# Kernel optimization log

Hardware: AMD Instinct MI355X
Metric: run time of the kernel (lower is better)

Reference implementation:

```python
import jax, jax.numpy as jnp
import numpy as np

B, T, C = 4, 2048, 1024
N_HEADS = 16
HEAD_DIM = C // N_HEADS


def setup_inputs() -> dict:
    key = jax.random.key(0)
    k1, k2, k3 = jax.random.split(key, 3)
    x = jax.random.normal(k1, (B, T, C), dtype=jnp.float32)
    w_qkv = jax.random.normal(k2, (C, 3 * C), dtype=jnp.float32) * (1.0 / np.sqrt(C))
    w_proj = jax.random.normal(k3, (C, C), dtype=jnp.float32) * (1.0 / np.sqrt(C))
    return {"x": x, "w_qkv": w_qkv, "w_proj": w_proj}


def reference(x, w_qkv, w_proj):
    b, t, c = x.shape
    qkv = x @ w_qkv                                  # [B,T,3C]
    q, k, v = jnp.split(qkv, 3, axis=-1)
    def split_heads(u):
        return u.reshape(b, t, N_HEADS, HEAD_DIM).transpose(0, 2, 1, 3)  # [B,H,T,D]
    q, k, v = split_heads(q), split_heads(k), split_heads(v)
    scale = 1.0 / np.sqrt(HEAD_DIM)
    att = jnp.einsum('bhqd,bhkd->bhqk', q, k) * scale   # [B,H,T,T]
    causal = jnp.tril(jnp.ones((t, t), dtype=bool))
    att = jnp.where(causal[None, None], att, -jnp.inf)
    att = jax.nn.softmax(att, axis=-1)
    out = jnp.einsum('bhqk,bhkd->bhqd', att, v)         # [B,H,T,D]
    out = out.transpose(0, 2, 1, 3).reshape(b, t, c)
    return out @ w_proj
```

## Files before the change

### kernel.cpp

```cpp
#include <hip/hip_runtime.h>
#include <hip/hip_bf16.h>
#include <stdint.h>

typedef __bf16 bf16_t;
typedef __bf16 bf16x4 __attribute__((ext_vector_type(4)));
typedef __bf16 bf16x8 __attribute__((ext_vector_type(8)));
typedef float  f32x4  __attribute__((ext_vector_type(4)));

#define B_    4
#define T_    2048
#define C_    1024
#define NH    16
#define HD    64
#define M_TOT (B_ * T_)

__device__ __forceinline__ void gload16(const void* g, void* l) {
    __builtin_amdgcn_global_load_lds(
        (const __attribute__((address_space(1))) uint32_t*)g,
        (__attribute__((address_space(3))) uint32_t*)l, 16, 0, 0);
}

__global__ void conv_x_kernel(const float* __restrict__ x, bf16_t* __restrict__ xb, int n4) {
    int i = blockIdx.x * blockDim.x + threadIdx.x;
    int stride = gridDim.x * blockDim.x;
    for (; i < n4; i += stride) {
        float4 v = reinterpret_cast<const float4*>(x)[i];
        union { bf16_t h[4]; uint2 u; } p;
        p.h[0] = (bf16_t)v.x; p.h[1] = (bf16_t)v.y;
        p.h[2] = (bf16_t)v.z; p.h[3] = (bf16_t)v.w;
        reinterpret_cast<uint2*>(xb)[i] = p.u;
    }
}

__global__ void transpose_w_kernel(const float* __restrict__ w, bf16_t* __restrict__ wt,
                                   int K, int N) {
    __shared__ float tile[32][33];
    int n0 = blockIdx.x * 32, k0 = blockIdx.y * 32;
    int tx = threadIdx.x, ty = threadIdx.y;
    #pragma unroll
    for (int i = 0; i < 32; i += 8)
        tile[ty + i][tx] = w[(size_t)(k0 + ty + i) * N + n0 + tx];
    __syncthreads();
    #pragma unroll
    for (int i = 0; i < 32; i += 8)
        wt[(size_t)(n0 + ty + i) * K + k0 + tx] = (bf16_t)tile[tx][ty + i];
}

#define QSCALE 0.18033688011112042f

#define LA0 0
#define LA1 16384
#define LB0 32768
#define LB1 49152

#define GST(ptr, rbase, base, kt) do { int k0_ = ((kt) << 6) & (K - 1);           \
    _Pragma("unroll") for (int c_ = 0; c_ < 4; ++c_) {                            \
        int li_ = tid + c_ * 256; int row_ = li_ >> 3;                            \
        int sw_ = (li_ & 7) ^ (row_ & 7);                                         \
        gload16(ptr + (size_t)((rbase) + row_) * K + k0_ + sw_ * 8,               \
                lds + (base) + li_ * 16); } } while (0)

#define GREAD(abase, bbase) do {                                                  \
    _Pragma("unroll") for (int mi_ = 0; mi_ < 4; ++mi_)                           \
        _Pragma("unroll") for (int kk_ = 0; kk_ < 2; ++kk_) {                     \
            int row_  = wm * 64 + mi_ * 16 + q16;                                 \
            int byte_ = (row_ * 128 + kk_ * 64 + g * 16) ^ ((row_ & 7) << 4);     \
            af[mi_ * 2 + kk_] = *reinterpret_cast<const bf16x8*>(lds + (abase) + byte_); } \
    _Pragma("unroll") for (int n_ = 0; n_ < 4; ++n_)                              \
        _Pragma("unroll") for (int kk_ = 0; kk_ < 2; ++kk_) {                     \
            int row_  = wn * 64 + n_ * 16 + q16;                                  \
            int byte_ = (row_ * 128 + kk_ * 64 + g * 16) ^ ((row_ & 7) << 4);     \
            bfr[n_ * 2 + kk_] = *reinterpret_cast<const bf16x8*>(lds + (bbase) + byte_); } } while (0)

#define GMFMA(milo) do { __builtin_amdgcn_s_setprio(1);                           \
    _Pragma("unroll") for (int mi_ = 0; mi_ < 2; ++mi_)                           \
        _Pragma("unroll") for (int kk_ = 0; kk_ < 2; ++kk_)                       \
            _Pragma("unroll") for (int n_ = 0; n_ < 4; ++n_)                      \
                acc[(milo) + mi_][n_] = __builtin_amdgcn_mfma_f32_16x16x32_bf16(  \
                    af[((milo) + mi_) * 2 + kk_], bfr[n_ * 2 + kk_],              \
                    acc[(milo) + mi_][n_], 0, 0, 0);                              \
    __builtin_amdgcn_s_setprio(0); } while (0)

template<int MODE>
__global__ __launch_bounds__(256, 2) void gemm_kernel(
    const bf16_t* __restrict__ A, const bf16_t* __restrict__ Bt,
    float* __restrict__ Cout,
    bf16_t* __restrict__ Qo, bf16_t* __restrict__ Ko, bf16_t* __restrict__ Vt,
    int M, int N, int K)
{
    __shared__ __align__(16) char lds[65536];
    const int tid  = threadIdx.x;
    const int lane = tid & 63;
    const int wid  = tid >> 6;
    const int wm   = wid >> 1, wn = wid & 1;
    const int q16  = lane & 15, g = lane >> 4;
    const int xcd = blockIdx.x & 7;
    const int i0  = blockIdx.x >> 3;
    const int mbase = (xcd * 8 + (i0 & 7)) * 128;
    const int nbase = (i0 >> 3) * 128;
    const int NITER = K >> 7;

    f32x4  acc[4][4] = {};
    bf16x8 af[8], bfr[8];

    GST(A, mbase, LA0, 0); GST(Bt, nbase, LB0, 0);
    GST(A, mbase, LA1, 1); GST(Bt, nbase, LB1, 1);
    asm volatile("s_waitcnt vmcnt(8)" ::: "memory");
    __builtin_amdgcn_s_barrier();
    __builtin_amdgcn_sched_barrier(0);

    #pragma unroll 1
    for (int i = 0; i < NITER; ++i) {
        GREAD(LA0, LB0);
        __builtin_amdgcn_s_barrier();
        asm volatile("s_waitcnt lgkmcnt(0)" ::: "memory");
        __builtin_amdgcn_sched_barrier(0);
        GMFMA(0);
        __builtin_amdgcn_s_barrier();
        GST(A, mbase, LA0, 2 * i + 2); GST(Bt, nbase, LB0, 2 * i + 2);
        __builtin_amdgcn_sched_barrier(0);
        GMFMA(2);
        asm volatile("s_waitcnt vmcnt(8)" ::: "memory");
        __builtin_amdgcn_s_barrier();
        GREAD(LA1, LB1);
        __builtin_amdgcn_s_barrier();
        asm volatile("s_waitcnt lgkmcnt(0)" ::: "memory");
        __builtin_amdgcn_sched_barrier(0);
        GMFMA(0);
        __builtin_amdgcn_s_barrier();
        GST(A, mbase, LA1, 2 * i + 3); GST(Bt, nbase, LB1, 2 * i + 3);
        __builtin_amdgcn_sched_barrier(0);
        GMFMA(2);
        asm volatile("s_waitcnt vmcnt(8)" ::: "memory");
        __builtin_amdgcn_s_barrier();
    }
    asm volatile("s_waitcnt vmcnt(0)" ::: "memory");

    #pragma unroll
    for (int mi = 0; mi < 4; ++mi) {
        #pragma unroll
        for (int n = 0; n < 4; ++n) {
            const int row0 = mbase + wm * 64 + mi * 16 + g * 4;
            const int col0 = nbase + wn * 64 + n * 16;
            if (MODE == 0) {
                #pragma unroll
                for (int r = 0; r < 4; ++r)
                    Cout[(size_t)(row0 + r) * N + col0 + q16] = acc[mi][n][r];
            } else {
                const int b = row0 >> 11, t0 = row0 & 2047;
                if (col0 < 1024) {
                    int h = col0 >> 6, d = (col0 & 63) + q16;
                    #pragma unroll
                    for (int r = 0; r < 4; ++r)
                        Qo[((size_t)(b * NH + h) * T_ + t0 + r) * HD + d] =
                            (bf16_t)(acc[mi][n][r] * QSCALE);
                } else if (col0 < 2048) {
                    int h = (col0 - 1024) >> 6, d = (col0 & 63) + q16;
                    #pragma unroll
                    for (int r = 0; r < 4; ++r)
                        Ko[((size_t)(b * NH + h) * T_ + t0 + r) * HD + d] =
                            (bf16_t)acc[mi][n][r];
                } else {
                    int h = (col0 - 2048) >> 6, d = (col0 & 63) + q16;
                    bf16x4 vv = { (bf16_t)acc[mi][n][0], (bf16_t)acc[mi][n][1],
                                  (bf16_t)acc[mi][n][2], (bf16_t)acc[mi][n][3] };
                    *reinterpret_cast<bf16x4*>(
                        Vt + ((size_t)(b * NH + h) * HD + d) * T_ + t0) = vv;
                }
            }
        }
    }
}

__global__ __launch_bounds__(256, 3) void attn_kernel(
    const bf16_t* __restrict__ Q, const bf16_t* __restrict__ K,
    const bf16_t* __restrict__ Vt, bf16_t* __restrict__ out)
{
    __shared__ __align__(16) char kvbuf[2][16384];
    __shared__ __align__(16) char plds[4][2048];
    const int tid  = threadIdx.x;
    const int lane = tid & 63;
    const int wid  = tid >> 6;
    const int g    = lane >> 4;
    const int q16  = lane & 15;

    const int bid = blockIdx.x;
    const int k   = bid >> 6;
    const int bh  = bid & 63;
    const int b   = bh >> 4, h = bh & 15;
    const int qt  = (k < 4) ? (15 - k) : (k < 8) ? (k + 4) : (k < 12) ? (k - 4) : (15 - k);

    const bf16_t* Qh = Q  + (size_t)bh * T_ * HD;
    const bf16_t* Kh = K  + (size_t)bh * T_ * HD;
    const bf16_t* Vh = Vt + (size_t)bh * HD * T_;
    char* myp = plds[wid];
    const int pswz = (q16 & 7) << 4;

    const int nt    = 2 * qt + 2;
    const int qbase = qt * 128 + wid * 32;
    const int qg0   = qbase + q16;
    const int qg1   = qbase + 16 + q16;

    int koff[4][2], pwoff[4], proff[2];
    #pragma unroll
    for (int t = 0; t < 4; ++t) {
        #pragma unroll
        for (int kk = 0; kk < 2; ++kk)
            koff[t][kk] = ((t * 16 + q16) * 128 + kk * 64 + g * 16) ^ pswz;
        pwoff[t] = (q16 * 128 + t * 32 + g * 8) ^ pswz;
    }
    proff[0] = (q16 * 128 + g * 16) ^ pswz;
    proff[1] = (q16 * 128 + 64 + g * 16) ^ pswz;

    const int li0 = tid,        row0 = li0 >> 3, sw0 = (li0 & 7) ^ (row0 & 7);
    const int li1 = tid + 256,  row1 = li1 >> 3, sw1 = (li1 & 7) ^ (row1 & 7);
    const bf16_t* kS0 = Kh + (size_t)row0 * HD + sw0 * 8;
    const bf16_t* kS1 = Kh + (size_t)row1 * HD + sw1 * 8;
    const bf16_t* vS0 = Vh + (size_t)row0 * T_ + sw0 * 8;
    const bf16_t* vS1 = Vh + (size_t)row1 * T_ + sw1 * 8;

#define STAGE2(buf) do {                                                          \
        gload16(kS0, (char*)(buf) + tid * 16);                                    \
        gload16(kS1, (char*)(buf) + 4096 + tid * 16);                             \
        gload16(vS0, (char*)(buf) + 8192 + tid * 16);                             \
        gload16(vS1, (char*)(buf) + 12288 + tid * 16);                            \
        kS0 += 4096; kS1 += 4096; vS0 += 64; vS1 += 64; } while (0)

    bf16x8 qf0[2], qf1[2];
    #pragma unroll
    for (int kk = 0; kk < 2; ++kk) {
        qf0[kk] = *reinterpret_cast<const bf16x8*>(Qh + (size_t)qg0 * HD + kk * 32 + g * 8);
        qf1[kk] = *reinterpret_cast<const bf16x8*>(Qh + (size_t)qg1 * HD + kk * 32 + g * 8);
    }

    f32x4 acc0[4] = {}, acc1[4] = {};
    float l0 = 0.f, l1 = 0.f;

#define ABODY(IT, CURB, NXTB) do {                                                \
    const int kv0 = (IT) << 6;                                                    \
    if ((IT) + 1 < nt) {                                                          \
        STAGE2(NXTB);                                                             \
        asm volatile("s_waitcnt vmcnt(4)" ::: "memory");                          \
    } else {                                                                      \
        asm volatile("s_waitcnt vmcnt(0)" ::: "memory");                          \
    }                                                                             \
    __builtin_amdgcn_s_barrier();                                                 \
    __builtin_amdgcn_sched_barrier(0);                                            \
    const char* Kl = (const char*)(CURB);                                         \
    const char* Vl = (const char*)(CURB) + 8192;                                  \
    f32x4 s0[4] = {}, s1[4] = {};                                                 \
    __builtin_amdgcn_s_setprio(1);                                                \
    _Pragma("unroll") for (int t = 0; t < 4; ++t)                                 \
        _Pragma("unroll") for (int kk = 0; kk < 2; ++kk) {                        \
            bf16x8 kf = *reinterpret_cast<const bf16x8*>(Kl + koff[t][kk]);       \
            s0[t] = __builtin_amdgcn_mfma_f32_16x16x32_bf16(kf, qf0[kk], s0[t], 0, 0, 0); \
            s1[t] = __builtin_amdgcn_mfma_f32_16x16x32_bf16(kf, qf1[kk], s1[t], 0, 0, 0); } \
    __builtin_amdgcn_s_setprio(0);                                                \
    if (kv0 + 63 > qbase) {                                                       \
        _Pragma("unroll") for (int t = 0; t < 4; ++t)                             \
            _Pragma("unroll") for (int r = 0; r < 4; ++r) {                       \
                int kv = kv0 + t * 16 + g * 4 + r;                                \
                if (kv > qg0) s0[t][r] = -1e30f;                                  \
                if (kv > qg1) s1[t][r] = -1e30f; } }                              \
                                  \
    _Pragma("unroll") for (int t = 0; t < 4; ++t) {                               \
        float p00 = exp2f(s0[t][0]), p01 = exp2f(s0[t][1]);                       \
        float p02 = exp2f(s0[t][2]), p03 = exp2f(s0[t][3]);                       \
        l0 += (p00 + p01) + (p02 + p03);                                          \
        bf16x4 pw0 = { (bf16_t)p00, (bf16_t)p01, (bf16_t)p02, (bf16_t)p03 };      \
        *reinterpret_cast<bf16x4*>(myp + pwoff[t]) = pw0; }                       \
    asm volatile("s_waitcnt lgkmcnt(0)" ::: "memory");                            \
    __builtin_amdgcn_sched_barrier(0);                                            \
    bf16x8 pf0[2];                                                                \
    _Pragma("unroll") for (int kk2 = 0; kk2 < 2; ++kk2)                           \
        pf0[kk2] = *reinterpret_cast<const bf16x8*>(myp + proff[kk2]);            \
    __builtin_amdgcn_s_setprio(1);                                                \
    _Pragma("unroll") for (int nf = 0; nf < 4; ++nf)                              \
        _Pragma("unroll") for (int kk2 = 0; kk2 < 2; ++kk2) {                     \
            bf16x8 vf = *reinterpret_cast<const bf16x8*>(Vl + koff[nf][kk2]);     \
            acc0[nf] = __builtin_amdgcn_mfma_f32_16x16x32_bf16(vf, pf0[kk2], acc0[nf], 0, 0, 0); } \
    __builtin_amdgcn_s_setprio(0);                                                \
     \
    _Pragma("unroll") for (int t = 0; t < 4; ++t) {                               \
        float p10 = exp2f(s1[t][0]), p11 = exp2f(s1[t][1]);                       \
        float p12 = exp2f(s1[t][2]), p13 = exp2f(s1[t][3]);                       \
        l1 += (p10 + p11) + (p12 + p13);                                          \
        bf16x4 pw1 = { (bf16_t)p10, (bf16_t)p11, (bf16_t)p12, (bf16_t)p13 };      \
        *reinterpret_cast<bf16x4*>(myp + pwoff[t]) = pw1; }                       \
    asm volatile("s_waitcnt lgkmcnt(0)" ::: "memory");                            \
    __builtin_amdgcn_sched_barrier(0);                                            \
    bf16x8 pf1[2];                                                                \
    _Pragma("unroll") for (int kk2 = 0; kk2 < 2; ++kk2)                           \
        pf1[kk2] = *reinterpret_cast<const bf16x8*>(myp + proff[kk2]);            \
    __builtin_amdgcn_s_setprio(1);                                                \
    _Pragma("unroll") for (int nf = 0; nf < 4; ++nf)                              \
        _Pragma("unroll") for (int kk2 = 0; kk2 < 2; ++kk2) {                     \
            bf16x8 vf = *reinterpret_cast<const bf16x8*>(Vl + koff[nf][kk2]);     \
            acc1[nf] = __builtin_amdgcn_mfma_f32_16x16x32_bf16(vf, pf1[kk2], acc1[nf], 0, 0, 0); } \
    __builtin_amdgcn_s_setprio(0);                                                \
    asm volatile("s_waitcnt lgkmcnt(0)" ::: "memory");                            \
    __builtin_amdgcn_s_barrier();                                                 \
} while (0)

    STAGE2(kvbuf[0]);
    #pragma unroll 1
    for (int it = 0; it < nt; it += 2) {
        ABODY(it,     kvbuf[0], kvbuf[1]);
        ABODY(it + 1, kvbuf[1], kvbuf[0]);
    }

    l0 += __shfl_xor(l0, 16, 64);
    l0 += __shfl_xor(l0, 32, 64);
    l1 += __shfl_xor(l1, 16, 64);
    l1 += __shfl_xor(l1, 32, 64);
    float inv0 = 1.f / l0, inv1 = 1.f / l1;
    #pragma unroll
    for (int nf = 0; nf < 4; ++nf) {
        bf16x4 ov0 = { (bf16_t)(acc0[nf][0] * inv0), (bf16_t)(acc0[nf][1] * inv0),
                       (bf16_t)(acc0[nf][2] * inv0), (bf16_t)(acc0[nf][3] * inv0) };
        *reinterpret_cast<bf16x4*>(
            out + (size_t)(b * T_ + qg0) * C_ + h * HD + nf * 16 + g * 4) = ov0;
        bf16x4 ov1 = { (bf16_t)(acc1[nf][0] * inv1), (bf16_t)(acc1[nf][1] * inv1),
                       (bf16_t)(acc1[nf][2] * inv1), (bf16_t)(acc1[nf][3] * inv1) };
        *reinterpret_cast<bf16x4*>(
            out + (size_t)(b * T_ + qg1) * C_ + h * HD + nf * 16 + g * 4) = ov1;
    }
#undef ABODY
#undef STAGE2
}

extern "C" void kernel_launch(void* const* d_in, const int* in_sizes, int n_in,
                              void* d_out, int out_size, void* d_ws, size_t ws_size,
                              hipStream_t stream) {
    const float* x      = (const float*)d_in[0];
    const float* w_qkv  = (const float*)d_in[1];
    const float* w_proj = (const float*)d_in[2];
    float* out = (float*)d_out;

    char* ws = (char*)d_ws;
    bf16_t* xb     = (bf16_t*)(ws);
    bf16_t* wqkvT  = (bf16_t*)(ws + 16777216);
    bf16_t* wprojT = (bf16_t*)(ws + 23068672);
    bf16_t* Qb     = (bf16_t*)(ws + 25165824);
    bf16_t* Kb     = (bf16_t*)(ws + 41943040);
    bf16_t* Vtb    = (bf16_t*)(ws + 58720256);
    bf16_t* attnb  = (bf16_t*)(ws + 75497472);

    conv_x_kernel<<<2048, 256, 0, stream>>>(x, xb, (B_ * T_ * C_) / 4);
    transpose_w_kernel<<<dim3(3 * C_ / 32, C_ / 32), dim3(32, 8), 0, stream>>>(w_qkv, wqkvT, C_, 3 * C_);
    transpose_w_kernel<<<dim3(C_ / 32, C_ / 32), dim3(32, 8), 0, stream>>>(w_proj, wprojT, C_, C_);

    gemm_kernel<1><<<1536, 256, 0, stream>>>(
        xb, wqkvT, nullptr, Qb, Kb, Vtb, M_TOT, 3 * C_, C_);

    attn_kernel<<<1024, 256, 0, stream>>>(Qb, Kb, Vtb, attnb);

    gemm_kernel<0><<<512, 256, 0, stream>>>(
        attnb, wprojT, out, nullptr, nullptr, nullptr, M_TOT, C_, C_);
}
```

Before: 162.9 us.

## Split long causal query tiles across two blocks with a combine kernel

Query tiles 8-15, which have the most key/value blocks under the causal mask, are now split into two halves of the KV range and run by separate blocks. Each half writes an unnormalized bf16 partial output and its row sums into a scratch buffer that reuses the xb workspace region, and a new combine kernel adds the halves and normalizes. A lookup table sets the block order to balance load across the grid, which grows from 1024 to 1536 blocks. The cost is an extra launch, extra global traffic for the partials, and rounding the partials to bf16. Merging by plain addition is exact only because no running max is used.

```diff
diff --git a/kernel.cpp b/kernel.cpp
--- a/kernel.cpp
+++ b/kernel.cpp
@@ -172,9 +172,17 @@
     }
 }
 
+#define PSLOT 16896
+
+__constant__ int8_t QT_TAB[24] = {15,15,7,6, 14,14,12,12, 13,13,11,5,
+                                  11,10,10,9, 8,3,9,4, 0,1,2,8};
+__constant__ int8_t MD_TAB[24] = {2,1,0,0, 2,1,2,1, 2,1,1,0,
+                                  2,2,1,1, 2,0,2,0, 0,0,0,1};
+
 __global__ __launch_bounds__(256, 3) void attn_kernel(
     const bf16_t* __restrict__ Q, const bf16_t* __restrict__ K,
-    const bf16_t* __restrict__ Vt, bf16_t* __restrict__ out)
+    const bf16_t* __restrict__ Vt, bf16_t* __restrict__ out,
+    char* __restrict__ pbuf)
 {
     __shared__ __align__(16) char kvbuf[2][16384];
     __shared__ __align__(16) char plds[4][2048];
@@ -185,10 +193,15 @@
     const int q16  = lane & 15;
 
     const int bid = blockIdx.x;
-    const int k   = bid >> 6;
+    const int cls = bid >> 6;
     const int bh  = bid & 63;
     const int b   = bh >> 4, h = bh & 15;
-    const int qt  = (k < 4) ? (15 - k) : (k < 8) ? (k + 4) : (k < 12) ? (k - 4) : (15 - k);
+    const int qt   = QT_TAB[cls];
+    const int mode = MD_TAB[cls];
+    const int ntot = 2 * qt + 2;
+    const int nt0  = (qt & 1) ? (qt + 1) : (qt + 2);
+    const int lo   = (mode == 2) ? nt0 : 0;
+    const int nt   = (mode == 0) ? ntot : (mode == 1 ? nt0 : ntot - nt0);
 
     const bf16_t* Qh = Q  + (size_t)bh * T_ * HD;
     const bf16_t* Kh = K  + (size_t)bh * T_ * HD;
@@ -196,7 +209,6 @@
     char* myp = plds[wid];
     const int pswz = (q16 & 7) << 4;
 
-    const int nt    = 2 * qt + 2;
     const int qbase = qt * 128 + wid * 32;
     const int qg0   = qbase + q16;
     const int qg1   = qbase + 16 + q16;
@@ -214,10 +226,11 @@
 
     const int li0 = tid,        row0 = li0 >> 3, sw0 = (li0 & 7) ^ (row0 & 7);
     const int li1 = tid + 256,  row1 = li1 >> 3, sw1 = (li1 & 7) ^ (row1 & 7);
-    const bf16_t* kS0 = Kh + (size_t)row0 * HD + sw0 * 8;
-    const bf16_t* kS1 = Kh + (size_t)row1 * HD + sw1 * 8;
-    const bf16_t* vS0 = Vh + (size_t)row0 * T_ + sw0 * 8;
-    const bf16_t* vS1 = Vh + (size_t)row1 * T_ + sw1 * 8;
+    const int kvlo = lo << 6;
+    const bf16_t* kS0 = Kh + (size_t)(kvlo + row0) * HD + sw0 * 8;
+    const bf16_t* kS1 = Kh + (size_t)(kvlo + row1) * HD + sw1 * 8;
+    const bf16_t* vS0 = Vh + (size_t)row0 * T_ + kvlo + sw0 * 8;
+    const bf16_t* vS1 = Vh + (size_t)row1 * T_ + kvlo + sw1 * 8;
 
 #define STAGE2(buf) do {                                                          \
         gload16(kS0, (char*)(buf) + tid * 16);                                    \
@@ -236,9 +249,9 @@
     f32x4 acc0[4] = {}, acc1[4] = {};
     float l0 = 0.f, l1 = 0.f;
 
-#define ABODY(IT, CURB, NXTB) do {                                                \
-    const int kv0 = (IT) << 6;                                                    \
-    if ((IT) + 1 < nt) {                                                          \
+#define ABODY(LIT, CURB, NXTB) do {                                               \
+    const int kv0 = (lo + (LIT)) << 6;                                            \
+    if ((LIT) + 1 < nt) {                                                         \
         STAGE2(NXTB);                                                             \
         asm volatile("s_waitcnt vmcnt(4)" ::: "memory");                          \
     } else {                                                                      \
@@ -262,7 +275,7 @@
                 int kv = kv0 + t * 16 + g * 4 + r;                                \
                 if (kv > qg0) s0[t][r] = -1e30f;                                  \
                 if (kv > qg1) s1[t][r] = -1e30f; } }                              \
-                                  \
+                                            \
     _Pragma("unroll") for (int t = 0; t < 4; ++t) {                               \
         float p00 = exp2f(s0[t][0]), p01 = exp2f(s0[t][1]);                       \
         float p02 = exp2f(s0[t][2]), p03 = exp2f(s0[t][3]);                       \
@@ -280,7 +293,7 @@
             bf16x8 vf = *reinterpret_cast<const bf16x8*>(Vl + koff[nf][kk2]);     \
             acc0[nf] = __builtin_amdgcn_mfma_f32_16x16x32_bf16(vf, pf0[kk2], acc0[nf], 0, 0, 0); } \
     __builtin_amdgcn_s_setprio(0);                                                \
-     \
+                              \
     _Pragma("unroll") for (int t = 0; t < 4; ++t) {                               \
         float p10 = exp2f(s1[t][0]), p11 = exp2f(s1[t][1]);                       \
         float p12 = exp2f(s1[t][2]), p13 = exp2f(s1[t][3]);                       \
@@ -313,20 +326,67 @@
     l0 += __shfl_xor(l0, 32, 64);
     l1 += __shfl_xor(l1, 16, 64);
     l1 += __shfl_xor(l1, 32, 64);
-    float inv0 = 1.f / l0, inv1 = 1.f / l1;
-    #pragma unroll
-    for (int nf = 0; nf < 4; ++nf) {
-        bf16x4 ov0 = { (bf16_t)(acc0[nf][0] * inv0), (bf16_t)(acc0[nf][1] * inv0),
-                       (bf16_t)(acc0[nf][2] * inv0), (bf16_t)(acc0[nf][3] * inv0) };
-        *reinterpret_cast<bf16x4*>(
-            out + (size_t)(b * T_ + qg0) * C_ + h * HD + nf * 16 + g * 4) = ov0;
-        bf16x4 ov1 = { (bf16_t)(acc1[nf][0] * inv1), (bf16_t)(acc1[nf][1] * inv1),
-                       (bf16_t)(acc1[nf][2] * inv1), (bf16_t)(acc1[nf][3] * inv1) };
-        *reinterpret_cast<bf16x4*>(
-            out + (size_t)(b * T_ + qg1) * C_ + h * HD + nf * 16 + g * 4) = ov1;
+
+    if (mode == 0) {
+        float inv0 = 1.f / l0, inv1 = 1.f / l1;
+        #pragma unroll
+        for (int nf = 0; nf < 4; ++nf) {
+            bf16x4 ov0 = { (bf16_t)(acc0[nf][0] * inv0), (bf16_t)(acc0[nf][1] * inv0),
+                           (bf16_t)(acc0[nf][2] * inv0), (bf16_t)(acc0[nf][3] * inv0) };
+            *reinterpret_cast<bf16x4*>(
+                out + (size_t)(b * T_ + qg0) * C_ + h * HD + nf * 16 + g * 4) = ov0;
+            bf16x4 ov1 = { (bf16_t)(acc1[nf][0] * inv1), (bf16_t)(acc1[nf][1] * inv1),
+                           (bf16_t)(acc1[nf][2] * inv1), (bf16_t)(acc1[nf][3] * inv1) };
+            *reinterpret_cast<bf16x4*>(
+                out + (size_t)(b * T_ + qg1) * C_ + h * HD + nf * 16 + g * 4) = ov1;
+        }
+    } else {
+        char* slot = pbuf + (size_t)((((bh << 3) + (qt - 8)) << 1) + (mode - 1)) * PSLOT;
+        const int r0 = wid * 32 + q16, r1 = r0 + 16;
+        #pragma unroll
+        for (int nf = 0; nf < 4; ++nf) {
+            bf16x4 a0 = { (bf16_t)acc0[nf][0], (bf16_t)acc0[nf][1],
+                          (bf16_t)acc0[nf][2], (bf16_t)acc0[nf][3] };
+            *reinterpret_cast<bf16x4*>(slot + r0 * 128 + (nf * 16 + g * 4) * 2) = a0;
+            bf16x4 a1 = { (bf16_t)acc1[nf][0], (bf16_t)acc1[nf][1],
+                          (bf16_t)acc1[nf][2], (bf16_t)acc1[nf][3] };
+            *reinterpret_cast<bf16x4*>(slot + r1 * 128 + (nf * 16 + g * 4) * 2) = a1;
+        }
+        if (g == 0) {
+            *reinterpret_cast<float*>(slot + 16384 + r0 * 4) = l0;
+            *reinterpret_cast<float*>(slot + 16384 + r1 * 4) = l1;
+        }
     }
 #undef ABODY
 #undef STAGE2
+}
+
+__global__ __launch_bounds__(256) void combine_kernel(
+    const char* __restrict__ pbuf, bf16_t* __restrict__ out)
+{
+    const int qtm8 = blockIdx.x;
+    const int bh   = blockIdx.y;
+    const int qt   = qtm8 + 8;
+    const int b = bh >> 4, h = bh & 15;
+    const char* s0 = pbuf + (size_t)((((bh << 3) + qtm8) << 1) + 0) * PSLOT;
+    const char* s1 = s0 + PSLOT;
+    const int t   = threadIdx.x;
+    const int row = t >> 1;
+    const int c0  = (t & 1) * 32;
+    float l = *reinterpret_cast<const float*>(s0 + 16384 + row * 4)
+            + *reinterpret_cast<const float*>(s1 + 16384 + row * 4);
+    float inv = 1.f / l;
+    bf16_t* op = out + (size_t)(b * T_ + qt * 128 + row) * C_ + h * HD + c0;
+    #pragma unroll
+    for (int j = 0; j < 8; ++j) {
+        bf16x4 a0 = *reinterpret_cast<const bf16x4*>(s0 + row * 128 + (c0 + j * 4) * 2);
+        bf16x4 a1 = *reinterpret_cast<const bf16x4*>(s1 + row * 128 + (c0 + j * 4) * 2);
+        bf16x4 o = { (bf16_t)(((float)a0[0] + (float)a1[0]) * inv),
+                     (bf16_t)(((float)a0[1] + (float)a1[1]) * inv),
+                     (bf16_t)(((float)a0[2] + (float)a1[2]) * inv),
+                     (bf16_t)(((float)a0[3] + (float)a1[3]) * inv) };
+        *reinterpret_cast<bf16x4*>(op + j * 4) = o;
+    }
 }
 
 extern "C" void kernel_launch(void* const* d_in, const int* in_sizes, int n_in,
@@ -345,6 +405,7 @@
     bf16_t* Kb     = (bf16_t*)(ws + 41943040);
     bf16_t* Vtb    = (bf16_t*)(ws + 58720256);
     bf16_t* attnb  = (bf16_t*)(ws + 75497472);
+    char*   pbuf   = ws;
 
     conv_x_kernel<<<2048, 256, 0, stream>>>(x, xb, (B_ * T_ * C_) / 4);
     transpose_w_kernel<<<dim3(3 * C_ / 32, C_ / 32), dim3(32, 8), 0, stream>>>(w_qkv, wqkvT, C_, 3 * C_);
@@ -353,7 +414,8 @@
     gemm_kernel<1><<<1536, 256, 0, stream>>>(
         xb, wqkvT, nullptr, Qb, Kb, Vtb, M_TOT, 3 * C_, C_);
 
-    attn_kernel<<<1024, 256, 0, stream>>>(Qb, Kb, Vtb, attnb);
+    attn_kernel<<<1536, 256, 0, stream>>>(Qb, Kb, Vtb, attnb, pbuf);
+    combine_kernel<<<dim3(8, 64), 256, 0, stream>>>(pbuf, attnb);
 
     gemm_kernel<0><<<512, 256, 0, stream>>>(
         attnb, wprojT, out, nullptr, nullptr, nullptr, M_TOT, C_, C_);
```

After: 171.6 us. 1.05x slower.
